# Kernel optimization log

Hardware: AMD Instinct MI355X
Metric: run time of the kernel (lower is better)

The kernel has to match this reference:

```python
import jax, jax.numpy as jnp
import numpy as np

EPS = 1e-6
H, HD = 16, 64

def layernorm(x):
    m = jnp.mean(x, -1, keepdims=True)
    v = jnp.mean((x - m) ** 2, -1, keepdims=True)
    return (x - m) * jax.lax.rsqrt(v + EPS)

def rmsnorm(x, w):
    return x * jax.lax.rsqrt(jnp.mean(x * x, -1, keepdims=True) + EPS) * w

def apply_rope(x, rope_emb):
    # x: [B,S,H,D], rope_emb: [S,1,1,D] with cos||sin halves
    half = rope_emb.shape[-1] // 2
    cos = jnp.transpose(rope_emb[..., :half], (1, 0, 2, 3))  # [1,S,1,half]
    sin = jnp.transpose(rope_emb[..., half:], (1, 0, 2, 3))
    x1, x2 = x[..., :half], x[..., half:]
    rotated = jnp.concatenate([-x2, x1], -1)
    return x * jnp.concatenate([cos, cos], -1) + rotated * jnp.concatenate([sin, sin], -1)

def attention(xq, ctx, wq, wk, wv, wo, qn, kn, rope_emb):
    B, S, _ = xq.shape
    M = ctx.shape[1]
    q = (xq @ wq.T).reshape(B, S, H, HD)
    k = (ctx @ wk.T).reshape(B, M, H, HD)
    v = (ctx @ wv.T).reshape(B, M, H, HD)
    q = rmsnorm(q, qn)
    k = rmsnorm(k, kn)
    if rope_emb is not None:  # self-attn only
        q = apply_rope(q, rope_emb)
        k = apply_rope(k, rope_emb)
    # explicit bf16 cast before SDPA, as in torch_attention_op
    qb, kb, vb = (t.astype(jnp.bfloat16) for t in (q, k, v))
    scale = 1.0 / np.sqrt(HD).astype(np.float32)
    scores = jnp.einsum('bqhd,bkhd->bhqk', qb, kb) * scale
    probs = jax.nn.softmax(scores.astype(jnp.float32), -1).astype(jnp.bfloat16)
    out = jnp.einsum('bhqk,bkhd->bqhd', probs, vb)  # [B,S,H,HD]
    out = out.reshape(B, S, H * HD).astype(jnp.float32)
    return out @ wo.T

def modulation(emb, w):
    y = jax.nn.silu(emb) @ w.T  # [B, 3D]
    shift, scale, gate = jnp.split(y, 3, axis=-1)
    return shift[:, None], scale[:, None], gate[:, None]  # [B,1,D]

def setup_inputs() -> dict:
    key = jax.random.key(0)
    B, S, D, M, DF = 1, 4096, 1024, 512, 4096
    ks = jax.random.split(key, 20)
    std_d = 1.0 / np.sqrt(D)
    inp = {
        'x': jax.random.normal(ks[0], (B, S, D), jnp.float32),
        'emb': jax.random.normal(ks[1], (B, D), jnp.float32),
        'crossattn_emb': jax.random.normal(ks[2], (B, M, D), jnp.float32),
        'sa_wq': jax.random.normal(ks[3], (D, D), jnp.float32) * std_d,
        'sa_wk': jax.random.normal(ks[4], (D, D), jnp.float32) * std_d,
        'sa_wv': jax.random.normal(ks[5], (D, D), jnp.float32) * std_d,
        'sa_wo': jax.random.normal(ks[6], (D, D), jnp.float32) * std_d,
        'sa_qn': jnp.ones((HD,), jnp.float32),
        'sa_kn': jnp.ones((HD,), jnp.float32),
        'ca_wq': jax.random.normal(ks[7], (D, D), jnp.float32) * std_d,
        'ca_wk': jax.random.normal(ks[8], (D, D), jnp.float32) * std_d,
        'ca_wv': jax.random.normal(ks[9], (D, D), jnp.float32) * std_d,
        'ca_wo': jax.random.normal(ks[10], (D, D), jnp.float32) * std_d,
        'ca_qn': jnp.ones((HD,), jnp.float32),
        'ca_kn': jnp.ones((HD,), jnp.float32),
        'mlp_w1': jax.random.normal(ks[11], (DF, D), jnp.float32) * std_d,
        'mlp_w2': jax.random.normal(ks[12], (D, DF), jnp.float32) * (1.0 / np.sqrt(DF)),
        'mod_sa_w': jax.random.normal(ks[13], (3 * D, D), jnp.float32) * 0.02,
        'mod_ca_w': jax.random.normal(ks[14], (3 * D, D), jnp.float32) * 0.02,
        'mod_mlp_w': jax.random.normal(ks[15], (3 * D, D), jnp.float32) * 0.02,
    }
    # RoPE table [S,1,1,HD]: first half cos, second half sin
    pos = jnp.arange(S, dtype=jnp.float32)
    inv_freq = 1.0 / (10000.0 ** (jnp.arange(0, HD // 2, dtype=jnp.float32) / (HD // 2)))
    ang = pos[:, None] * inv_freq[None, :]  # [S, HD/2]
    inp['rope_emb'] = jnp.concatenate([jnp.cos(ang), jnp.sin(ang)], -1)[:, None, None, :]
    return inp

def reference(x, emb, crossattn_emb, rope_emb, sa_wq, sa_wk, sa_wv, sa_wo, sa_qn, sa_kn,
              ca_wq, ca_wk, ca_wv, ca_wo, ca_qn, ca_kn, mlp_w1, mlp_w2,
              mod_sa_w, mod_ca_w, mod_mlp_w):
    # self-attn with adaln modulation
    sh, sc, g = modulation(emb, mod_sa_w)
    h = layernorm(x) * (1.0 + sc) + sh
    x = x + g * attention(h, h, sa_wq, sa_wk, sa_wv, sa_wo, sa_qn, sa_kn, rope_emb)
    # cross-attn
    sh, sc, g = modulation(emb, mod_ca_w)
    h = layernorm(x) * (1.0 + sc) + sh
    x = x + g * attention(h, crossattn_emb, ca_wq, ca_wk, ca_wv, ca_wo, ca_qn, ca_kn, None)
    # mlp
    sh, sc, g = modulation(emb, mod_mlp_w)
    h = layernorm(x) * (1.0 + sc) + sh
    x = x + g * (jax.nn.gelu(h @ mlp_w1.T, approximate=False) @ mlp_w2.T)
    return x
```

## Files before the change

kernel.cpp:

```cpp
#include <hip/hip_runtime.h>
#include <hip/hip_bf16.h>

typedef __attribute__((ext_vector_type(8))) __bf16 bf16x8;
typedef __attribute__((ext_vector_type(4))) float f32x4;
typedef __attribute__((ext_vector_type(4))) unsigned short us4;

__device__ __forceinline__ unsigned short f2bf(float f){
  union { float f; unsigned int u; } a; a.f = f;
  unsigned int r = 0x7fffu + ((a.u >> 16) & 1u);
  return (unsigned short)((a.u + r) >> 16);
}

__device__ __forceinline__ unsigned int cvt_pk_bf16(float lo, float hi){
  unsigned int d;
  asm("v_cvt_pk_bf16_f32 %0, %1, %2" : "=v"(d) : "v"(lo), "v"(hi));
  return d;
}

__device__ __forceinline__ float exp2_hw(float x){
  float d;
  asm("v_exp_f32 %0, %1" : "=v"(d) : "v"(x));
  return d;
}

__device__ __forceinline__ void gload_lds16(const unsigned short* g, void* l){
  __builtin_amdgcn_global_load_lds(
      (const __attribute__((address_space(1))) void*)g,
      (__attribute__((address_space(3))) void*)l, 16, 0, 0);
}

__global__ __launch_bounds__(256) void cast_kernel(const float* __restrict__ in,
                                                   unsigned short* __restrict__ out, int n4){
  int i = blockIdx.x * 256 + threadIdx.x;
  if (i >= n4) return;
  float4 v = ((const float4*)in)[i];
  us4 o; o.x = f2bf(v.x); o.y = f2bf(v.y); o.z = f2bf(v.z); o.w = f2bf(v.w);
  ((us4*)out)[i] = o;
}

__global__ __launch_bounds__(256) void modulation_kernel(const float* __restrict__ emb,
    const float* __restrict__ w0, const float* __restrict__ w1, const float* __restrict__ w2,
    float* __restrict__ out){
  int gw = blockIdx.x * 4 + (threadIdx.x >> 6);
  int lane = threadIdx.x & 63;
  int mat = gw / 3072, row = gw % 3072;
  const float* w = (mat == 0) ? w0 : (mat == 1 ? w1 : w2);
  float acc = 0.f;
  for (int i = lane; i < 1024; i += 64){
    float e = emb[i];
    float s = e / (1.f + expf(-e));
    acc += s * w[row * 1024 + i];
  }
  #pragma unroll
  for (int m = 32; m >= 1; m >>= 1) acc += __shfl_xor(acc, m, 64);
  if (lane == 0) out[mat * 3072 + row] = acc;
}

__global__ __launch_bounds__(256) void ln_mod_kernel(const float* __restrict__ x,
    const float* __restrict__ mod, unsigned short* __restrict__ h){
  int row = blockIdx.x, t = threadIdx.x;
  const float* xr = x + (size_t)row * 1024;
  float4 v = ((const float4*)xr)[t];
  float s = v.x + v.y + v.z + v.w;
  #pragma unroll
  for (int m = 32; m >= 1; m >>= 1) s += __shfl_xor(s, m, 64);
  __shared__ float red[4], red2[4];
  int wid = t >> 6, lane = t & 63;
  if (lane == 0) red[wid] = s;
  __syncthreads();
  float mean = (red[0] + red[1] + red[2] + red[3]) * (1.f / 1024.f);
  float dx = v.x - mean, dy = v.y - mean, dz = v.z - mean, dw = v.w - mean;
  float s2 = dx*dx + dy*dy + dz*dz + dw*dw;
  #pragma unroll
  for (int m = 32; m >= 1; m >>= 1) s2 += __shfl_xor(s2, m, 64);
  if (lane == 0) red2[wid] = s2;
  __syncthreads();
  float var = (red2[0] + red2[1] + red2[2] + red2[3]) * (1.f / 1024.f);
  float rs = rsqrtf(var + 1e-6f);
  int c = t * 4;
  us4 o;
  o.x = f2bf(dx * rs * (1.f + mod[1024 + c    ]) + mod[c    ]);
  o.y = f2bf(dy * rs * (1.f + mod[1024 + c + 1]) + mod[c + 1]);
  o.z = f2bf(dz * rs * (1.f + mod[1024 + c + 2]) + mod[c + 2]);
  o.w = f2bf(dw * rs * (1.f + mod[1024 + c + 3]) + mod[c + 3]);
  ((us4*)(h + (size_t)row * 1024))[t] = o;
}

template<int ROPE>
__global__ __launch_bounds__(256) void qk_post_kernel(const float* __restrict__ qin,
    const float* __restrict__ nw, const float* __restrict__ rope,
    unsigned short* __restrict__ qout, int S){
  int gw = blockIdx.x * 4 + (threadIdx.x >> 6);
  int lane = threadIdx.x & 63;
  int s = gw >> 4, h = gw & 15;
  float v = qin[(size_t)s * 1024 + h * 64 + lane];
  float ss = v * v;
  #pragma unroll
  for (int m = 32; m >= 1; m >>= 1) ss += __shfl_xor(ss, m, 64);
  float val = v * rsqrtf(ss * (1.f / 64.f) + 1e-6f) * nw[lane];
  if (ROPE){
    float partner = __shfl_xor(val, 32, 64);
    float cs = rope[s * 64 + (lane & 31)];
    float sn = rope[s * 64 + 32 + (lane & 31)];
    val = (lane < 32) ? (val * cs - partner * sn) : (val * cs + partner * sn);
  }
  qout[((size_t)h * S + s) * 64 + lane] = f2bf(val);
}

__global__ __launch_bounds__(256) void vt_kernel(const float* __restrict__ Vf,
    unsigned short* __restrict__ Vt, int S){
  int stile = blockIdx.x, h = blockIdx.y;
  __shared__ unsigned short tile[64 * 66];
  int t = threadIdx.x;
  #pragma unroll
  for (int i = 0; i < 16; i++){
    int e = i * 256 + t;
    int srow = e >> 6, d = e & 63;
    tile[d * 66 + srow] = f2bf(Vf[(size_t)(stile * 64 + srow) * 1024 + h * 64 + d]);
  }
  __syncthreads();
  #pragma unroll
  for (int i = 0; i < 16; i++){
    int e = i * 256 + t;
    int d = e >> 6, scol = e & 63;
    Vt[((size_t)h * 64 + d) * S + stile * 64 + scol] = tile[d * 66 + scol];
  }
}

template<int EPI>
__global__ __launch_bounds__(256) void gemm_bt_kernel(
    const unsigned short* __restrict__ A, const unsigned short* __restrict__ W,
    int M, int N, int K,
    float* __restrict__ outF, unsigned short* __restrict__ outB,
    const float* __restrict__ resid, const float* __restrict__ gate){
  __shared__ short As[128 * 64];
  __shared__ short Bs[128 * 64];
  const int t = threadIdx.x, wid = t >> 6, lane = t & 63;
  const int r = lane & 15, g = lane >> 4;
  const int brow = blockIdx.y * 128, bcol = blockIdx.x * 128;
  const int wr = wid >> 1, wc = wid & 1;
  f32x4 acc[4][4] = {};
  const int nkt = K >> 6;
  for (int kt = 0; kt < nkt; ++kt){
    const int k0 = kt << 6;
    #pragma unroll
    for (int i = 0; i < 4; i++){
      int chunk = wid * 4 + i;
      int rowi = chunk * 8 + (lane >> 3);
      int lce = ((lane & 7) * 8) ^ ((rowi & 7) << 3);
      gload_lds16(A + (size_t)(brow + rowi) * K + k0 + lce, (void*)(As + chunk * 512));
      gload_lds16(W + (size_t)(bcol + rowi) * K + k0 + lce, (void*)(Bs + chunk * 512));
    }
    __syncthreads();
    #pragma unroll
    for (int kk = 0; kk < 2; kk++){
      bf16x8 af[4], bfr[4];
      #pragma unroll
      for (int m = 0; m < 4; m++){
        int ar = wr * 64 + m * 16 + r;
        af[m] = *(const bf16x8*)(As + ar * 64 + ((kk * 32 + g * 8) ^ ((ar & 7) << 3)));
      }
      #pragma unroll
      for (int n = 0; n < 4; n++){
        int br = wc * 64 + n * 16 + r;
        bfr[n] = *(const bf16x8*)(Bs + br * 64 + ((kk * 32 + g * 8) ^ ((br & 7) << 3)));
      }
      #pragma unroll
      for (int m = 0; m < 4; m++)
        #pragma unroll
        for (int n = 0; n < 4; n++)
          acc[m][n] = __builtin_amdgcn_mfma_f32_16x16x32_bf16(af[m], bfr[n], acc[m][n], 0, 0, 0);
    }
    __syncthreads();
  }
  #pragma unroll
  for (int m = 0; m < 4; m++){
    #pragma unroll
    for (int n = 0; n < 4; n++){
      int col = bcol + wc * 64 + n * 16 + r;
      #pragma unroll
      for (int j = 0; j < 4; j++){
        int rowj = brow + wr * 64 + m * 16 + g * 4 + j;
        float v = acc[m][n][j];
        if (EPI == 0){
          outF[(size_t)rowj * N + col] = v;
        } else if (EPI == 2){
          float gl = 0.5f * v * (1.f + erff(v * 0.70710678118654752f));
          outB[(size_t)rowj * N + col] = f2bf(gl);
        } else if (EPI == 4){
          outF[(size_t)(col >> 10) * 4194304 + (size_t)rowj * 1024 + (col & 1023)] = v;
        } else {
          outF[(size_t)rowj * N + col] = resid[(size_t)rowj * N + col] + gate[col] * v;
        }
      }
    }
  }
}

template<int EPI>
__global__ __launch_bounds__(256) void gemm_bt64_kernel(
    const unsigned short* __restrict__ A, const unsigned short* __restrict__ W,
    int M, int N, int K,
    float* __restrict__ outF, unsigned short* __restrict__ outB,
    const float* __restrict__ resid, const float* __restrict__ gate){
  __shared__ short As[64 * 64];
  __shared__ short Bs[128 * 64];
  const int t = threadIdx.x, wid = t >> 6, lane = t & 63;
  const int r = lane & 15, g = lane >> 4;
  const int brow = blockIdx.y * 64, bcol = blockIdx.x * 128;
  f32x4 acc[4][2] = {};
  const int nkt = K >> 6;
  const int sr = lane >> 3;
  const int lce = ((lane & 7) * 8) ^ ((sr & 7) << 3);
  for (int kt = 0; kt < nkt; ++kt){
    const int k0 = kt << 6;
    #pragma unroll
    for (int i = 0; i < 2; i++){
      int chunk = wid * 2 + i;
      gload_lds16(A + (size_t)(brow + chunk * 8 + sr) * K + k0 + lce, (void*)(As + chunk * 512));
    }
    #pragma unroll
    for (int i = 0; i < 4; i++){
      int chunk = wid * 4 + i;
      gload_lds16(W + (size_t)(bcol + chunk * 8 + sr) * K + k0 + lce, (void*)(Bs + chunk * 512));
    }
    __syncthreads();
    #pragma unroll
    for (int kk = 0; kk < 2; kk++){
      bf16x8 af[4], bfr[2];
      #pragma unroll
      for (int m = 0; m < 4; m++){
        int ar = m * 16 + r;
        af[m] = *(const bf16x8*)(As + ar * 64 + ((kk * 32 + g * 8) ^ ((ar & 7) << 3)));
      }
      #pragma unroll
      for (int n = 0; n < 2; n++){
        int br = wid * 32 + n * 16 + r;
        bfr[n] = *(const bf16x8*)(Bs + br * 64 + ((kk * 32 + g * 8) ^ ((br & 7) << 3)));
      }
      #pragma unroll
      for (int m = 0; m < 4; m++)
        #pragma unroll
        for (int n = 0; n < 2; n++)
          acc[m][n] = __builtin_amdgcn_mfma_f32_16x16x32_bf16(af[m], bfr[n], acc[m][n], 0, 0, 0);
    }
    __syncthreads();
  }
  #pragma unroll
  for (int m = 0; m < 4; m++){
    #pragma unroll
    for (int n = 0; n < 2; n++){
      int col = bcol + wid * 32 + n * 16 + r;
      #pragma unroll
      for (int j = 0; j < 4; j++){
        int rowj = brow + m * 16 + g * 4 + j;
        float v = acc[m][n][j];
        if (EPI == 0){
          outF[(size_t)rowj * N + col] = v;
        } else if (EPI == 4){
          outF[(size_t)(col >> 10) * 4194304 + (size_t)rowj * 1024 + (col & 1023)] = v;
        } else {
          outF[(size_t)rowj * N + col] = resid[(size_t)rowj * N + col] + gate[col] * v;
        }
      }
    }
  }
}

__global__ __launch_bounds__(256) void attn_kernel(
    const unsigned short* __restrict__ Qb, const unsigned short* __restrict__ Kb,
    const unsigned short* __restrict__ Vtg, unsigned short* __restrict__ Out,
    int Sq, int Skv){
  __shared__ short Ks[2][4096];
  __shared__ short Vs[2][4096];
  __shared__ unsigned short Ps[4][2048];
  const int t = threadIdx.x, wid = t >> 6, lane = t & 63;
  const int r = lane & 15, g = lane >> 4;
  const int bid = blockIdx.x;
  const int slot = bid >> 3;
  const int h = (bid & 7) * 2 + (slot >> 5);
  const int qblk = slot & 31;
  const int qbase = qblk * 128 + wid * 32;
  const float SC = 0.18033688f;
  const float MS = 12.0f;

  const int srow0 = wid * 16 + (lane >> 3);
  const int scol  = ((lane & 7) * 8) ^ (((lane >> 3) & 7) << 3);
  const unsigned short* kSrc0 = Kb + ((size_t)h * Skv + srow0) * 64 + scol;
  const unsigned short* kSrc1 = kSrc0 + 8 * 64;
  const unsigned short* vSrc0 = Vtg + ((size_t)h * 64 + srow0) * Skv + scol;
  const unsigned short* vSrc1 = vSrc0 + (size_t)8 * Skv;

  bf16x8 qf[2][2];
  #pragma unroll
  for (int qt = 0; qt < 2; qt++){
    const unsigned short* qp = Qb + ((size_t)h * Sq + qbase + qt * 16 + r) * 64 + g * 8;
    qf[qt][0] = *(const bf16x8*)qp;
    qf[qt][1] = *(const bf16x8*)(qp + 32);
  }
  f32x4 o[2][4] = {};
  f32x4 lacc[2] = {};

  const int nkv = Skv >> 6;
  gload_lds16(kSrc0, (void*)&Ks[0][(wid * 2 + 0) * 512]);
  gload_lds16(kSrc1, (void*)&Ks[0][(wid * 2 + 1) * 512]);
  gload_lds16(vSrc0, (void*)&Vs[0][(wid * 2 + 0) * 512]);
  gload_lds16(vSrc1, (void*)&Vs[0][(wid * 2 + 1) * 512]);
  asm volatile("s_waitcnt vmcnt(0)" ::: "memory");
  __syncthreads();

  int cur = 0;
  for (int it = 0; it < nkv; ++it){
    if (it + 1 < nkv){
      int nxt = cur ^ 1;
      size_t ko = (size_t)(it + 1) << 12;
      size_t vo = (size_t)(it + 1) << 6;
      gload_lds16(kSrc0 + ko, (void*)&Ks[nxt][(wid * 2 + 0) * 512]);
      gload_lds16(kSrc1 + ko, (void*)&Ks[nxt][(wid * 2 + 1) * 512]);
      gload_lds16(vSrc0 + vo, (void*)&Vs[nxt][(wid * 2 + 0) * 512]);
      gload_lds16(vSrc1 + vo, (void*)&Vs[nxt][(wid * 2 + 1) * 512]);
    }
    const short* kb = &Ks[cur][0];
    const short* vb = &Vs[cur][0];

    f32x4 pT[2][4];
    __builtin_amdgcn_s_setprio(1);
    #pragma unroll
    for (int kt = 0; kt < 4; kt++){
      int kr = kt * 16 + r;
      bf16x8 k0 = *(const bf16x8*)(kb + kr * 64 + ((g * 8) ^ ((kr & 7) << 3)));
      bf16x8 k1 = *(const bf16x8*)(kb + kr * 64 + ((32 + g * 8) ^ ((kr & 7) << 3)));
      #pragma unroll
      for (int qt = 0; qt < 2; qt++){
        f32x4 a = {};
        a = __builtin_amdgcn_mfma_f32_16x16x32_bf16(k0, qf[qt][0], a, 0, 0, 0);
        a = __builtin_amdgcn_mfma_f32_16x16x32_bf16(k1, qf[qt][1], a, 0, 0, 0);
        pT[qt][kt] = a;
      }
    }
    __builtin_amdgcn_s_setprio(0);

    #pragma unroll
    for (int qt = 0; qt < 2; qt++){
      unsigned short* pw = &Ps[wid][(qt * 16 + r) * 64];
      int rx = (r & 7) << 3;
      #pragma unroll
      for (int kt = 0; kt < 4; kt++){
        f32x4 pe;
        #pragma unroll
        for (int e = 0; e < 4; e++) pe[e] = exp2_hw(fmaf(pT[qt][kt][e], SC, -MS));
        lacc[qt] += pe;
        unsigned int w0 = cvt_pk_bf16(pe[0], pe[1]);
        unsigned int w1 = cvt_pk_bf16(pe[2], pe[3]);
        *(uint2*)(pw + ((kt * 16 + g * 4) ^ rx)) = make_uint2(w0, w1);
      }
    }

    __builtin_amdgcn_s_setprio(1);
    #pragma unroll
    for (int qt = 0; qt < 2; qt++){
      const unsigned short* pw = &Ps[wid][(qt * 16 + r) * 64];
      int rx = (r & 7) << 3;
      bf16x8 pf0 = *(const bf16x8*)(pw + ((g * 8) ^ rx));
      bf16x8 pf1 = *(const bf16x8*)(pw + ((32 + g * 8) ^ rx));
      #pragma unroll
      for (int dj = 0; dj < 4; dj++){
        int vrow = dj * 16 + r;
        bf16x8 v0 = *(const bf16x8*)(vb + vrow * 64 + ((g * 8) ^ ((vrow & 7) << 3)));
        bf16x8 v1 = *(const bf16x8*)(vb + vrow * 64 + ((32 + g * 8) ^ ((vrow & 7) << 3)));
        o[qt][dj] = __builtin_amdgcn_mfma_f32_16x16x32_bf16(pf0, v0, o[qt][dj], 0, 0, 0);
        o[qt][dj] = __builtin_amdgcn_mfma_f32_16x16x32_bf16(pf1, v1, o[qt][dj], 0, 0, 0);
      }
    }
    __builtin_amdgcn_s_setprio(0);

    asm volatile("s_waitcnt vmcnt(0)" ::: "memory");
    __syncthreads();
    cur ^= 1;
  }

  #pragma unroll
  for (int qt = 0; qt < 2; qt++){
    float s = (lacc[qt][0] + lacc[qt][1]) + (lacc[qt][2] + lacc[qt][3]);
    s += __shfl_xor(s, 16, 64);
    s += __shfl_xor(s, 32, 64);
    float inv = 1.f / s;
    int sb = lane & 48;
    #pragma unroll
    for (int j = 0; j < 4; j++){
      float aj = __shfl(inv, sb + g * 4 + j, 64);
      int qrow = qbase + qt * 16 + g * 4 + j;
      #pragma unroll
      for (int dj = 0; dj < 4; dj++)
        Out[(size_t)qrow * 1024 + h * 64 + dj * 16 + r] = f2bf(o[qt][dj][j] * aj);
    }
  }
}

extern "C" void kernel_launch(void* const* d_in, const int* in_sizes, int n_in,
                              void* d_out, int out_size, void* d_ws, size_t ws_size,
                              hipStream_t stream){
  (void)n_in; (void)out_size;
  const float* x   = (const float*)d_in[0];
  const float* emb = (const float*)d_in[1];
  const float* ctx = (const float*)d_in[2];
  int wb = 3, ri = 20;
  if (in_sizes[3] == 4096 * 64) { ri = 3; wb = 4; }
  const float* rope  = (const float*)d_in[ri];
  const float* sa_wq = (const float*)d_in[wb + 0];
  const float* sa_wk = (const float*)d_in[wb + 1];
  const float* sa_wv = (const float*)d_in[wb + 2];
  const float* sa_wo = (const float*)d_in[wb + 3];
  const float* sa_qn = (const float*)d_in[wb + 4];
  const float* sa_kn = (const float*)d_in[wb + 5];
  const float* ca_wq = (const float*)d_in[wb + 6];
  const float* ca_wk = (const float*)d_in[wb + 7];
  const float* ca_wv = (const float*)d_in[wb + 8];
  const float* ca_wo = (const float*)d_in[wb + 9];
  const float* ca_qn = (const float*)d_in[wb + 10];
  const float* ca_kn = (const float*)d_in[wb + 11];
  const float* w1    = (const float*)d_in[wb + 12];
  const float* w2    = (const float*)d_in[wb + 13];
  const float* msa   = (const float*)d_in[wb + 14];
  const float* mca   = (const float*)d_in[wb + 15];
  const float* mmlp  = (const float*)d_in[wb + 16];

  char* ws = (char*)d_ws;
  const size_t MB = 1u << 20;
  if (ws_size < 114 * MB) return;
  unsigned short* wq_sa = (unsigned short*)(ws + 0 * MB);
  unsigned short* wk_sa = (unsigned short*)(ws + 2 * MB);
  unsigned short* wv_sa = (unsigned short*)(ws + 4 * MB);
  unsigned short* wo_sa = (unsigned short*)(ws + 6 * MB);
  unsigned short* wq_ca = (unsigned short*)(ws + 8 * MB);
  unsigned short* wk_ca = (unsigned short*)(ws + 10 * MB);
  unsigned short* wv_ca = (unsigned short*)(ws + 12 * MB);
  unsigned short* wo_ca = (unsigned short*)(ws + 14 * MB);
  unsigned short* w1bf  = (unsigned short*)(ws + 16 * MB);
  unsigned short* w2bf  = (unsigned short*)(ws + 24 * MB);
  unsigned short* ctxbf = (unsigned short*)(ws + 32 * MB);
  float*          modv  = (float*)(ws + 33 * MB);
  unsigned short* hbf   = (unsigned short*)(ws + 34 * MB);
  unsigned short* qbf   = (unsigned short*)(ws + 42 * MB);
  unsigned short* kbf   = (unsigned short*)(ws + 50 * MB);
  unsigned short* aobf  = (unsigned short*)(ws + 58 * MB);
  float*          qf32  = (float*)(ws + 66 * MB);
  float*          kf32  = (float*)(ws + 82 * MB);
  float*          vf32  = (float*)(ws + 98 * MB);
  unsigned short* vtb   = (unsigned short*)(ws + 82 * MB);
  unsigned short* midbf = (unsigned short*)(ws + 66 * MB);
  float* xcur = (float*)d_out;

  hipMemcpyAsync(d_out, x, (size_t)4096 * 1024 * 4, hipMemcpyDeviceToDevice, stream);

  auto cast = [&](const float* src, unsigned short* dst, int n){
    cast_kernel<<<(n / 4 + 255) / 256, 256, 0, stream>>>(src, dst, n / 4);
  };
  cast(sa_wq, wq_sa, 1024 * 1024);
  cast(sa_wk, wk_sa, 1024 * 1024);
  cast(sa_wv, wv_sa, 1024 * 1024);
  cast(sa_wo, wo_sa, 1024 * 1024);
  cast(ca_wq, wq_ca, 1024 * 1024);
  cast(ca_wk, wk_ca, 1024 * 1024);
  cast(ca_wv, wv_ca, 1024 * 1024);
  cast(ca_wo, wo_ca, 1024 * 1024);
  cast(w1, w1bf, 4096 * 1024);
  cast(w2, w2bf, 4096 * 1024);
  cast(ctx, ctxbf, 512 * 1024);
  modulation_kernel<<<2304, 256, 0, stream>>>(emb, msa, mca, mmlp, modv);

  ln_mod_kernel<<<4096, 256, 0, stream>>>(xcur, modv + 0 * 3072, hbf);
  gemm_bt_kernel<4><<<dim3(24, 32), 256, 0, stream>>>(hbf, wq_sa, 4096, 3072, 1024, qf32, nullptr, nullptr, nullptr);
  qk_post_kernel<1><<<16384, 256, 0, stream>>>(qf32, sa_qn, rope, qbf, 4096);
  qk_post_kernel<1><<<16384, 256, 0, stream>>>(kf32, sa_kn, rope, kbf, 4096);
  vt_kernel<<<dim3(64, 16), 256, 0, stream>>>(vf32, vtb, 4096);
  attn_kernel<<<512, 256, 0, stream>>>(qbf, kbf, vtb, aobf, 4096, 4096);
  gemm_bt64_kernel<3><<<dim3(8, 64), 256, 0, stream>>>(aobf, wo_sa, 4096, 1024, 1024, xcur, nullptr, xcur, modv + 0 * 3072 + 2048);

  ln_mod_kernel<<<4096, 256, 0, stream>>>(xcur, modv + 1 * 3072, hbf);
  gemm_bt64_kernel<0><<<dim3(8, 64), 256, 0, stream>>>(hbf, wq_ca, 4096, 1024, 1024, qf32, nullptr, nullptr, nullptr);
  gemm_bt64_kernel<4><<<dim3(16, 8), 256, 0, stream>>>(ctxbf, wk_ca, 512, 2048, 1024, kf32, nullptr, nullptr, nullptr);
  qk_post_kernel<0><<<16384, 256, 0, stream>>>(qf32, ca_qn, nullptr, qbf, 4096);
  qk_post_kernel<0><<<2048, 256, 0, stream>>>(kf32, ca_kn, nullptr, kbf, 512);
  vt_kernel<<<dim3(8, 16), 256, 0, stream>>>(vf32, vtb, 512);
  attn_kernel<<<512, 256, 0, stream>>>(qbf, kbf, vtb, aobf, 4096, 512);
  gemm_bt64_kernel<3><<<dim3(8, 64), 256, 0, stream>>>(aobf, wo_ca, 4096, 1024, 1024, xcur, nullptr, xcur, modv + 1 * 3072 + 2048);

  ln_mod_kernel<<<4096, 256, 0, stream>>>(xcur, modv + 2 * 3072, hbf);
  gemm_bt_kernel<2><<<dim3(32, 32), 256, 0, stream>>>(hbf, w1bf, 4096, 4096, 1024, nullptr, midbf, nullptr, nullptr);
  gemm_bt64_kernel<3><<<dim3(8, 64), 256, 0, stream>>>(midbf, w2bf, 4096, 1024, 4096, xcur, nullptr, xcur, modv + 2 * 3072 + 2048);
}
```

Baseline: 471.2 us.

## Halve attention query tile, batch weight casts into one launch, drop x copy

The attention kernel now gives each wave 16 query rows instead of 32 and launches twice as many blocks, which raises parallelism and occupancy on the MI355X but doubles K/V tile loads per query. The eleven separate cast launches become one kernel that looks up each job's range from a block-offset table. The initial device-to-device copy of x into the output is removed: the first layernorm and the residual add read x directly and write the result into the output buffer.

```diff
diff --git a/kernel.cpp b/kernel.cpp
--- a/kernel.cpp
+++ b/kernel.cpp
@@ -29,13 +29,21 @@
       (__attribute__((address_space(3))) void*)l, 16, 0, 0);
 }
 
-__global__ __launch_bounds__(256) void cast_kernel(const float* __restrict__ in,
-                                                   unsigned short* __restrict__ out, int n4){
-  int i = blockIdx.x * 256 + threadIdx.x;
-  if (i >= n4) return;
-  float4 v = ((const float4*)in)[i];
+struct CastJobs {
+  const float* src[11];
+  unsigned short* dst[11];
+  int blkStart[12];
+};
+
+__global__ __launch_bounds__(256) void cast_all_kernel(CastJobs jobs){
+  int bid = blockIdx.x;
+  int j = 0;
+  #pragma unroll
+  for (int i = 0; i < 11; i++) j += (bid >= jobs.blkStart[i + 1]) ? 1 : 0;
+  int i4 = (bid - jobs.blkStart[j]) * 256 + threadIdx.x;
+  float4 v = ((const float4*)jobs.src[j])[i4];
   us4 o; o.x = f2bf(v.x); o.y = f2bf(v.y); o.z = f2bf(v.z); o.w = f2bf(v.w);
-  ((us4*)out)[i] = o;
+  ((us4*)jobs.dst[j])[i4] = o;
 }
 
 __global__ __launch_bounds__(256) void modulation_kernel(const float* __restrict__ emb,
@@ -273,14 +281,14 @@
     int Sq, int Skv){
   __shared__ short Ks[2][4096];
   __shared__ short Vs[2][4096];
-  __shared__ unsigned short Ps[4][2048];
+  __shared__ unsigned short Ps[4][1024];
   const int t = threadIdx.x, wid = t >> 6, lane = t & 63;
   const int r = lane & 15, g = lane >> 4;
   const int bid = blockIdx.x;
   const int slot = bid >> 3;
-  const int h = (bid & 7) * 2 + (slot >> 5);
-  const int qblk = slot & 31;
-  const int qbase = qblk * 128 + wid * 32;
+  const int h = (bid & 7) * 2 + (slot >> 6);
+  const int qblk = slot & 63;
+  const int qbase = qblk * 64 + wid * 16;
   const float SC = 0.18033688f;
   const float MS = 12.0f;
 
@@ -291,15 +299,14 @@
   const unsigned short* vSrc0 = Vtg + ((size_t)h * 64 + srow0) * Skv + scol;
   const unsigned short* vSrc1 = vSrc0 + (size_t)8 * Skv;
 
-  bf16x8 qf[2][2];
-  #pragma unroll
-  for (int qt = 0; qt < 2; qt++){
-    const unsigned short* qp = Qb + ((size_t)h * Sq + qbase + qt * 16 + r) * 64 + g * 8;
-    qf[qt][0] = *(const bf16x8*)qp;
-    qf[qt][1] = *(const bf16x8*)(qp + 32);
-  }
-  f32x4 o[2][4] = {};
-  f32x4 lacc[2] = {};
+  bf16x8 qf0, qf1;
+  {
+    const unsigned short* qp = Qb + ((size_t)h * Sq + qbase + r) * 64 + g * 8;
+    qf0 = *(const bf16x8*)qp;
+    qf1 = *(const bf16x8*)(qp + 32);
+  }
+  f32x4 o[4] = {};
+  f32x4 lacc = {};
 
   const int nkv = Skv >> 6;
   gload_lds16(kSrc0, (void*)&Ks[0][(wid * 2 + 0) * 512]);
@@ -323,33 +330,29 @@
     const short* kb = &Ks[cur][0];
     const short* vb = &Vs[cur][0];
 
-    f32x4 pT[2][4];
+    f32x4 pT[4];
     __builtin_amdgcn_s_setprio(1);
     #pragma unroll
     for (int kt = 0; kt < 4; kt++){
       int kr = kt * 16 + r;
       bf16x8 k0 = *(const bf16x8*)(kb + kr * 64 + ((g * 8) ^ ((kr & 7) << 3)));
       bf16x8 k1 = *(const bf16x8*)(kb + kr * 64 + ((32 + g * 8) ^ ((kr & 7) << 3)));
-      #pragma unroll
-      for (int qt = 0; qt < 2; qt++){
-        f32x4 a = {};
-        a = __builtin_amdgcn_mfma_f32_16x16x32_bf16(k0, qf[qt][0], a, 0, 0, 0);
-        a = __builtin_amdgcn_mfma_f32_16x16x32_bf16(k1, qf[qt][1], a, 0, 0, 0);
-        pT[qt][kt] = a;
-      }
+      f32x4 a = {};
+      a = __builtin_amdgcn_mfma_f32_16x16x32_bf16(k0, qf0, a, 0, 0, 0);
+      a = __builtin_amdgcn_mfma_f32_16x16x32_bf16(k1, qf1, a, 0, 0, 0);
+      pT[kt] = a;
     }
     __builtin_amdgcn_s_setprio(0);
 
-    #pragma unroll
-    for (int qt = 0; qt < 2; qt++){
-      unsigned short* pw = &Ps[wid][(qt * 16 + r) * 64];
+    {
+      unsigned short* pw = &Ps[wid][r * 64];
       int rx = (r & 7) << 3;
       #pragma unroll
       for (int kt = 0; kt < 4; kt++){
         f32x4 pe;
         #pragma unroll
-        for (int e = 0; e < 4; e++) pe[e] = exp2_hw(fmaf(pT[qt][kt][e], SC, -MS));
-        lacc[qt] += pe;
+        for (int e = 0; e < 4; e++) pe[e] = exp2_hw(fmaf(pT[kt][e], SC, -MS));
+        lacc += pe;
         unsigned int w0 = cvt_pk_bf16(pe[0], pe[1]);
         unsigned int w1 = cvt_pk_bf16(pe[2], pe[3]);
         *(uint2*)(pw + ((kt * 16 + g * 4) ^ rx)) = make_uint2(w0, w1);
@@ -357,9 +360,8 @@
     }
 
     __builtin_amdgcn_s_setprio(1);
-    #pragma unroll
-    for (int qt = 0; qt < 2; qt++){
-      const unsigned short* pw = &Ps[wid][(qt * 16 + r) * 64];
+    {
+      const unsigned short* pw = &Ps[wid][r * 64];
       int rx = (r & 7) << 3;
       bf16x8 pf0 = *(const bf16x8*)(pw + ((g * 8) ^ rx));
       bf16x8 pf1 = *(const bf16x8*)(pw + ((32 + g * 8) ^ rx));
@@ -368,8 +370,8 @@
         int vrow = dj * 16 + r;
         bf16x8 v0 = *(const bf16x8*)(vb + vrow * 64 + ((g * 8) ^ ((vrow & 7) << 3)));
         bf16x8 v1 = *(const bf16x8*)(vb + vrow * 64 + ((32 + g * 8) ^ ((vrow & 7) << 3)));
-        o[qt][dj] = __builtin_amdgcn_mfma_f32_16x16x32_bf16(pf0, v0, o[qt][dj], 0, 0, 0);
-        o[qt][dj] = __builtin_amdgcn_mfma_f32_16x16x32_bf16(pf1, v1, o[qt][dj], 0, 0, 0);
+        o[dj] = __builtin_amdgcn_mfma_f32_16x16x32_bf16(pf0, v0, o[dj], 0, 0, 0);
+        o[dj] = __builtin_amdgcn_mfma_f32_16x16x32_bf16(pf1, v1, o[dj], 0, 0, 0);
       }
     }
     __builtin_amdgcn_s_setprio(0);
@@ -379,9 +381,8 @@
     cur ^= 1;
   }
 
-  #pragma unroll
-  for (int qt = 0; qt < 2; qt++){
-    float s = (lacc[qt][0] + lacc[qt][1]) + (lacc[qt][2] + lacc[qt][3]);
+  {
+    float s = (lacc[0] + lacc[1]) + (lacc[2] + lacc[3]);
     s += __shfl_xor(s, 16, 64);
     s += __shfl_xor(s, 32, 64);
     float inv = 1.f / s;
@@ -389,10 +390,10 @@
     #pragma unroll
     for (int j = 0; j < 4; j++){
       float aj = __shfl(inv, sb + g * 4 + j, 64);
-      int qrow = qbase + qt * 16 + g * 4 + j;
+      int qrow = qbase + g * 4 + j;
       #pragma unroll
       for (int dj = 0; dj < 4; dj++)
-        Out[(size_t)qrow * 1024 + h * 64 + dj * 16 + r] = f2bf(o[qt][dj][j] * aj);
+        Out[(size_t)qrow * 1024 + h * 64 + dj * 16 + r] = f2bf(o[dj][j] * aj);
     }
   }
 }
@@ -451,31 +452,26 @@
   unsigned short* midbf = (unsigned short*)(ws + 66 * MB);
   float* xcur = (float*)d_out;
 
-  hipMemcpyAsync(d_out, x, (size_t)4096 * 1024 * 4, hipMemcpyDeviceToDevice, stream);
-
-  auto cast = [&](const float* src, unsigned short* dst, int n){
-    cast_kernel<<<(n / 4 + 255) / 256, 256, 0, stream>>>(src, dst, n / 4);
-  };
-  cast(sa_wq, wq_sa, 1024 * 1024);
-  cast(sa_wk, wk_sa, 1024 * 1024);
-  cast(sa_wv, wv_sa, 1024 * 1024);
-  cast(sa_wo, wo_sa, 1024 * 1024);
-  cast(ca_wq, wq_ca, 1024 * 1024);
-  cast(ca_wk, wk_ca, 1024 * 1024);
-  cast(ca_wv, wv_ca, 1024 * 1024);
-  cast(ca_wo, wo_ca, 1024 * 1024);
-  cast(w1, w1bf, 4096 * 1024);
-  cast(w2, w2bf, 4096 * 1024);
-  cast(ctx, ctxbf, 512 * 1024);
+  CastJobs cj;
+  const float* srcs[11] = {sa_wq, sa_wk, sa_wv, sa_wo, ca_wq, ca_wk, ca_wv, ca_wo, w1, w2, ctx};
+  unsigned short* dsts[11] = {wq_sa, wk_sa, wv_sa, wo_sa, wq_ca, wk_ca, wv_ca, wo_ca, w1bf, w2bf, ctxbf};
+  int n4s[11] = {262144, 262144, 262144, 262144, 262144, 262144, 262144, 262144, 1048576, 1048576, 131072};
+  int cum = 0;
+  for (int i = 0; i < 11; i++){
+    cj.src[i] = srcs[i]; cj.dst[i] = dsts[i];
+    cj.blkStart[i] = cum; cum += n4s[i] / 256;
+  }
+  cj.blkStart[11] = cum;
+  cast_all_kernel<<<cum, 256, 0, stream>>>(cj);
   modulation_kernel<<<2304, 256, 0, stream>>>(emb, msa, mca, mmlp, modv);
 
-  ln_mod_kernel<<<4096, 256, 0, stream>>>(xcur, modv + 0 * 3072, hbf);
+  ln_mod_kernel<<<4096, 256, 0, stream>>>(x, modv + 0 * 3072, hbf);
   gemm_bt_kernel<4><<<dim3(24, 32), 256, 0, stream>>>(hbf, wq_sa, 4096, 3072, 1024, qf32, nullptr, nullptr, nullptr);
   qk_post_kernel<1><<<16384, 256, 0, stream>>>(qf32, sa_qn, rope, qbf, 4096);
   qk_post_kernel<1><<<16384, 256, 0, stream>>>(kf32, sa_kn, rope, kbf, 4096);
   vt_kernel<<<dim3(64, 16), 256, 0, stream>>>(vf32, vtb, 4096);
-  attn_kernel<<<512, 256, 0, stream>>>(qbf, kbf, vtb, aobf, 4096, 4096);
-  gemm_bt64_kernel<3><<<dim3(8, 64), 256, 0, stream>>>(aobf, wo_sa, 4096, 1024, 1024, xcur, nullptr, xcur, modv + 0 * 3072 + 2048);
+  attn_kernel<<<1024, 256, 0, stream>>>(qbf, kbf, vtb, aobf, 4096, 4096);
+  gemm_bt64_kernel<3><<<dim3(8, 64), 256, 0, stream>>>(aobf, wo_sa, 4096, 1024, 1024, xcur, nullptr, x, modv + 0 * 3072 + 2048);
 
   ln_mod_kernel<<<4096, 256, 0, stream>>>(xcur, modv + 1 * 3072, hbf);
   gemm_bt64_kernel<0><<<dim3(8, 64), 256, 0, stream>>>(hbf, wq_ca, 4096, 1024, 1024, qf32, nullptr, nullptr, nullptr);
@@ -483,7 +479,7 @@
   qk_post_kernel<0><<<16384, 256, 0, stream>>>(qf32, ca_qn, nullptr, qbf, 4096);
   qk_post_kernel<0><<<2048, 256, 0, stream>>>(kf32, ca_kn, nullptr, kbf, 512);
   vt_kernel<<<dim3(8, 16), 256, 0, stream>>>(vf32, vtb, 512);
-  attn_kernel<<<512, 256, 0, stream>>>(qbf, kbf, vtb, aobf, 4096, 512);
+  attn_kernel<<<1024, 256, 0, stream>>>(qbf, kbf, vtb, aobf, 4096, 512);
   gemm_bt64_kernel<3><<<dim3(8, 64), 256, 0, stream>>>(aobf, wo_ca, 4096, 1024, 1024, xcur, nullptr, xcur, modv + 1 * 3072 + 2048);
 
   ln_mod_kernel<<<4096, 256, 0, stream>>>(xcur, modv + 2 * 3072, hbf);
```

Result: faster. 453.1 us (-3.8%).

## Batch casts, merge qk_post launches, drop x copy, split-K the MLP down GEMM

Applied to the files above, without the earlier changes.

Merges the eleven per-tensor cast launches into one job-table kernel and merges the Q and K norm/rope launches into one grid, cutting launch overhead. Removes the initial device-to-device copy of x by reading x directly in the first layernorm and as the residual of the first output projection. The MLP down projection (K=4096) is split into two K-halves written to partial buffers, then a separate reduce kernel adds the gated sum into the residual. This adds 32 MB of partial writes and reads in exchange for twice as many workgroups on the long-K GEMM.

```diff
diff --git a/kernel.cpp b/kernel.cpp
--- a/kernel.cpp
+++ b/kernel.cpp
@@ -29,13 +29,21 @@
       (__attribute__((address_space(3))) void*)l, 16, 0, 0);
 }
 
-__global__ __launch_bounds__(256) void cast_kernel(const float* __restrict__ in,
-                                                   unsigned short* __restrict__ out, int n4){
-  int i = blockIdx.x * 256 + threadIdx.x;
-  if (i >= n4) return;
-  float4 v = ((const float4*)in)[i];
+struct CastJobs {
+  const float* src[11];
+  unsigned short* dst[11];
+  int blkStart[12];
+};
+
+__global__ __launch_bounds__(256) void cast_all_kernel(CastJobs jobs){
+  int bid = blockIdx.x;
+  int j = 0;
+  #pragma unroll
+  for (int i = 0; i < 11; i++) j += (bid >= jobs.blkStart[i + 1]) ? 1 : 0;
+  int i4 = (bid - jobs.blkStart[j]) * 256 + threadIdx.x;
+  float4 v = ((const float4*)jobs.src[j])[i4];
   us4 o; o.x = f2bf(v.x); o.y = f2bf(v.y); o.z = f2bf(v.z); o.w = f2bf(v.w);
-  ((us4*)out)[i] = o;
+  ((us4*)jobs.dst[j])[i4] = o;
 }
 
 __global__ __launch_bounds__(256) void modulation_kernel(const float* __restrict__ emb,
@@ -87,13 +95,20 @@
 }
 
 template<int ROPE>
-__global__ __launch_bounds__(256) void qk_post_kernel(const float* __restrict__ qin,
-    const float* __restrict__ nw, const float* __restrict__ rope,
-    unsigned short* __restrict__ qout, int S){
-  int gw = blockIdx.x * 4 + (threadIdx.x >> 6);
+__global__ __launch_bounds__(256) void qk_post2_kernel(
+    const float* __restrict__ qin, const float* __restrict__ qnw,
+    const float* __restrict__ kin, const float* __restrict__ knw,
+    const float* __restrict__ rope,
+    unsigned short* __restrict__ qout, unsigned short* __restrict__ kout,
+    int Sq, int Sk, int qblocks){
+  int bid = blockIdx.x;
+  const float* in; const float* nw; unsigned short* out; int S;
+  if (bid < qblocks){ in = qin; nw = qnw; out = qout; S = Sq; }
+  else { in = kin; nw = knw; out = kout; S = Sk; bid -= qblocks; }
+  int gw = bid * 4 + (threadIdx.x >> 6);
   int lane = threadIdx.x & 63;
   int s = gw >> 4, h = gw & 15;
-  float v = qin[(size_t)s * 1024 + h * 64 + lane];
+  float v = in[(size_t)s * 1024 + h * 64 + lane];
   float ss = v * v;
   #pragma unroll
   for (int m = 32; m >= 1; m >>= 1) ss += __shfl_xor(ss, m, 64);
@@ -104,7 +119,7 @@
     float sn = rope[s * 64 + 32 + (lane & 31)];
     val = (lane < 32) ? (val * cs - partner * sn) : (val * cs + partner * sn);
   }
-  qout[((size_t)h * S + s) * 64 + lane] = f2bf(val);
+  out[((size_t)h * S + s) * 64 + lane] = f2bf(val);
 }
 
 __global__ __launch_bounds__(256) void vt_kernel(const float* __restrict__ Vf,
@@ -265,6 +280,85 @@
       }
     }
   }
+}
+
+__global__ __launch_bounds__(256) void gemm_bt64_sk_kernel(
+    const unsigned short* __restrict__ A, const unsigned short* __restrict__ W,
+    int M, int N, int K, float* __restrict__ outP){
+  __shared__ short As[64 * 64];
+  __shared__ short Bs[128 * 64];
+  const int t = threadIdx.x, wid = t >> 6, lane = t & 63;
+  const int r = lane & 15, g = lane >> 4;
+  const int brow = blockIdx.y * 64, bcol = blockIdx.x * 128;
+  const int zk = blockIdx.z;
+  const int koff = zk * (K >> 1);
+  float* out = outP + (size_t)zk * 4194304;
+  f32x4 acc[4][2] = {};
+  const int nkt = K >> 7;
+  const int sr = lane >> 3;
+  const int lce = ((lane & 7) * 8) ^ ((sr & 7) << 3);
+  for (int kt = 0; kt < nkt; ++kt){
+    const int k0 = koff + (kt << 6);
+    #pragma unroll
+    for (int i = 0; i < 2; i++){
+      int chunk = wid * 2 + i;
+      gload_lds16(A + (size_t)(brow + chunk * 8 + sr) * K + k0 + lce, (void*)(As + chunk * 512));
+    }
+    #pragma unroll
+    for (int i = 0; i < 4; i++){
+      int chunk = wid * 4 + i;
+      gload_lds16(W + (size_t)(bcol + chunk * 8 + sr) * K + k0 + lce, (void*)(Bs + chunk * 512));
+    }
+    __syncthreads();
+    #pragma unroll
+    for (int kk = 0; kk < 2; kk++){
+      bf16x8 af[4], bfr[2];
+      #pragma unroll
+      for (int m = 0; m < 4; m++){
+        int ar = m * 16 + r;
+        af[m] = *(const bf16x8*)(As + ar * 64 + ((kk * 32 + g * 8) ^ ((ar & 7) << 3)));
+      }
+      #pragma unroll
+      for (int n = 0; n < 2; n++){
+        int br = wid * 32 + n * 16 + r;
+        bfr[n] = *(const bf16x8*)(Bs + br * 64 + ((kk * 32 + g * 8) ^ ((br & 7) << 3)));
+      }
+      #pragma unroll
+      for (int m = 0; m < 4; m++)
+        #pragma unroll
+        for (int n = 0; n < 2; n++)
+          acc[m][n] = __builtin_amdgcn_mfma_f32_16x16x32_bf16(af[m], bfr[n], acc[m][n], 0, 0, 0);
+    }
+    __syncthreads();
+  }
+  #pragma unroll
+  for (int m = 0; m < 4; m++){
+    #pragma unroll
+    for (int n = 0; n < 2; n++){
+      int col = bcol + wid * 32 + n * 16 + r;
+      #pragma unroll
+      for (int j = 0; j < 4; j++){
+        int rowj = brow + m * 16 + g * 4 + j;
+        out[(size_t)rowj * N + col] = acc[m][n][j];
+      }
+    }
+  }
+}
+
+__global__ __launch_bounds__(256) void reduce_gg_kernel(const float* __restrict__ p0,
+    const float* __restrict__ p1, const float* __restrict__ gate, float* __restrict__ xio){
+  int i4 = blockIdx.x * 256 + threadIdx.x;
+  float4 a = ((const float4*)p0)[i4];
+  float4 b = ((const float4*)p1)[i4];
+  float4 rr = ((const float4*)xio)[i4];
+  int col = (i4 * 4) & 1023;
+  float4 gv = *(const float4*)&gate[col];
+  float4 o;
+  o.x = rr.x + gv.x * (a.x + b.x);
+  o.y = rr.y + gv.y * (a.y + b.y);
+  o.z = rr.z + gv.z * (a.z + b.z);
+  o.w = rr.w + gv.w * (a.w + b.w);
+  ((float4*)xio)[i4] = o;
 }
 
 __global__ __launch_bounds__(256) void attn_kernel(
@@ -449,44 +543,40 @@
   float*          vf32  = (float*)(ws + 98 * MB);
   unsigned short* vtb   = (unsigned short*)(ws + 82 * MB);
   unsigned short* midbf = (unsigned short*)(ws + 66 * MB);
+  float*          mp0   = (float*)(ws + 34 * MB);
+  float*          mp1   = (float*)(ws + 50 * MB);
   float* xcur = (float*)d_out;
 
-  hipMemcpyAsync(d_out, x, (size_t)4096 * 1024 * 4, hipMemcpyDeviceToDevice, stream);
-
-  auto cast = [&](const float* src, unsigned short* dst, int n){
-    cast_kernel<<<(n / 4 + 255) / 256, 256, 0, stream>>>(src, dst, n / 4);
-  };
-  cast(sa_wq, wq_sa, 1024 * 1024);
-  cast(sa_wk, wk_sa, 1024 * 1024);
-  cast(sa_wv, wv_sa, 1024 * 1024);
-  cast(sa_wo, wo_sa, 1024 * 1024);
-  cast(ca_wq, wq_ca, 1024 * 1024);
-  cast(ca_wk, wk_ca, 1024 * 1024);
-  cast(ca_wv, wv_ca, 1024 * 1024);
-  cast(ca_wo, wo_ca, 1024 * 1024);
-  cast(w1, w1bf, 4096 * 1024);
-  cast(w2, w2bf, 4096 * 1024);
-  cast(ctx, ctxbf, 512 * 1024);
+  CastJobs cj;
+  const float* srcs[11] = {sa_wq, sa_wk, sa_wv, sa_wo, ca_wq, ca_wk, ca_wv, ca_wo, w1, w2, ctx};
+  unsigned short* dsts[11] = {wq_sa, wk_sa, wv_sa, wo_sa, wq_ca, wk_ca, wv_ca, wo_ca, w1bf, w2bf, ctxbf};
+  int n4s[11] = {262144, 262144, 262144, 262144, 262144, 262144, 262144, 262144, 1048576, 1048576, 131072};
+  int cum = 0;
+  for (int i = 0; i < 11; i++){
+    cj.src[i] = srcs[i]; cj.dst[i] = dsts[i];
+    cj.blkStart[i] = cum; cum += n4s[i] / 256;
+  }
+  cj.blkStart[11] = cum;
+  cast_all_kernel<<<cum, 256, 0, stream>>>(cj);
   modulation_kernel<<<2304, 256, 0, stream>>>(emb, msa, mca, mmlp, modv);
 
-  ln_mod_kernel<<<4096, 256, 0, stream>>>(xcur, modv + 0 * 3072, hbf);
+  ln_mod_kernel<<<4096, 256, 0, stream>>>(x, modv + 0 * 3072, hbf);
   gemm_bt_kernel<4><<<dim3(24, 32), 256, 0, stream>>>(hbf, wq_sa, 4096, 3072, 1024, qf32, nullptr, nullptr, nullptr);
-  qk_post_kernel<1><<<16384, 256, 0, stream>>>(qf32, sa_qn, rope, qbf, 4096);
-  qk_post_kernel<1><<<16384, 256, 0, stream>>>(kf32, sa_kn, rope, kbf, 4096);
+  qk_post2_kernel<1><<<32768, 256, 0, stream>>>(qf32, sa_qn, kf32, sa_kn, rope, qbf, kbf, 4096, 4096, 16384);
   vt_kernel<<<dim3(64, 16), 256, 0, stream>>>(vf32, vtb, 4096);
   attn_kernel<<<512, 256, 0, stream>>>(qbf, kbf, vtb, aobf, 4096, 4096);
-  gemm_bt64_kernel<3><<<dim3(8, 64), 256, 0, stream>>>(aobf, wo_sa, 4096, 1024, 1024, xcur, nullptr, xcur, modv + 0 * 3072 + 2048);
+  gemm_bt64_kernel<3><<<dim3(8, 64), 256, 0, stream>>>(aobf, wo_sa, 4096, 1024, 1024, xcur, nullptr, x, modv + 0 * 3072 + 2048);
 
   ln_mod_kernel<<<4096, 256, 0, stream>>>(xcur, modv + 1 * 3072, hbf);
   gemm_bt64_kernel<0><<<dim3(8, 64), 256, 0, stream>>>(hbf, wq_ca, 4096, 1024, 1024, qf32, nullptr, nullptr, nullptr);
   gemm_bt64_kernel<4><<<dim3(16, 8), 256, 0, stream>>>(ctxbf, wk_ca, 512, 2048, 1024, kf32, nullptr, nullptr, nullptr);
-  qk_post_kernel<0><<<16384, 256, 0, stream>>>(qf32, ca_qn, nullptr, qbf, 4096);
-  qk_post_kernel<0><<<2048, 256, 0, stream>>>(kf32, ca_kn, nullptr, kbf, 512);
+  qk_post2_kernel<0><<<18432, 256, 0, stream>>>(qf32, ca_qn, kf32, ca_kn, nullptr, qbf, kbf, 4096, 512, 16384);
   vt_kernel<<<dim3(8, 16), 256, 0, stream>>>(vf32, vtb, 512);
   attn_kernel<<<512, 256, 0, stream>>>(qbf, kbf, vtb, aobf, 4096, 512);
   gemm_bt64_kernel<3><<<dim3(8, 64), 256, 0, stream>>>(aobf, wo_ca, 4096, 1024, 1024, xcur, nullptr, xcur, modv + 1 * 3072 + 2048);
 
   ln_mod_kernel<<<4096, 256, 0, stream>>>(xcur, modv + 2 * 3072, hbf);
   gemm_bt_kernel<2><<<dim3(32, 32), 256, 0, stream>>>(hbf, w1bf, 4096, 4096, 1024, nullptr, midbf, nullptr, nullptr);
-  gemm_bt64_kernel<3><<<dim3(8, 64), 256, 0, stream>>>(midbf, w2bf, 4096, 1024, 4096, xcur, nullptr, xcur, modv + 2 * 3072 + 2048);
-}
+  gemm_bt64_sk_kernel<<<dim3(8, 64, 2), 256, 0, stream>>>(midbf, w2bf, 4096, 1024, 4096, mp0);
+  reduce_gg_kernel<<<4096, 256, 0, stream>>>(mp0, mp1, modv + 2 * 3072 + 2048, xcur);
+}
```

After: 441.5 us. -6.3%, faster.
